# Optimization experiments

Hardware: AMD Instinct MI355X
Metric: run time of the kernel (lower is better)

The kernel has to match this reference:

```python
import jax, jax.numpy as jnp
import numpy as np

B, S, D = 8, 1024, 512          # batch, seq_len, embed_dim
H = 8                            # num_heads
KD = D                           # key_dim = embed_dim (per source)
DM = H * KD                      # internal d_model = 4096
FF = 2048                        # dense_dim
EPS = 1e-3                       # keras LayerNormalization default epsilon


def glorot(key, shape):
    fan_in, fan_out = shape[0], shape[1]
    lim = np.sqrt(6.0 / (fan_in + fan_out)).astype(np.float32)
    return jax.random.uniform(key, shape, jnp.float32, -lim, lim)


def setup_inputs() -> dict:
    key = jax.random.key(0)
    ks = jax.random.split(key, 8)
    return {
        "inputs": jax.random.normal(ks[0], (B, S, D), jnp.float32),
        "w_q": glorot(ks[1], (D, DM)), "b_q": jnp.zeros((DM,), jnp.float32),
        "w_k": glorot(ks[2], (D, DM)), "b_k": jnp.zeros((DM,), jnp.float32),
        "w_v": glorot(ks[3], (D, DM)), "b_v": jnp.zeros((DM,), jnp.float32),
        "w_o": glorot(ks[4], (DM, D)), "b_o": jnp.zeros((D,), jnp.float32),
        "w1": glorot(ks[5], (D, FF)), "b1": jnp.zeros((FF,), jnp.float32),
        "w2": glorot(ks[6], (FF, D)), "b2": jnp.zeros((D,), jnp.float32),
        "g1": jnp.ones((D,), jnp.float32), "beta1": jnp.zeros((D,), jnp.float32),
        "g2": jnp.ones((D,), jnp.float32), "beta2": jnp.zeros((D,), jnp.float32),
    }


def _layernorm(x, gamma, beta):
    mu = jnp.mean(x, axis=-1, keepdims=True)
    var = jnp.mean(jnp.square(x - mu), axis=-1, keepdims=True)
    return (x - mu) * jax.lax.rsqrt(var + EPS) * gamma + beta


def reference(inputs, w_q, b_q, w_k, b_k, w_v, b_v, w_o, b_o,
              w1, b1, w2, b2, g1, beta1, g2, beta2):
    # --- custom multi-head self-attention ---
    q = (inputs @ w_q + b_q).reshape(B, S, H, KD)   # [B,S,H,KD]
    k = (inputs @ w_k + b_k).reshape(B, S, H, KD)
    v = (inputs @ w_v + b_v).reshape(B, S, H, KD)
    scale = jnp.sqrt(jnp.float32(KD))
    scores = jnp.einsum("bqhd,bkhd->bhqk", q, k) / scale   # [B,H,S,S]
    attn = jax.nn.softmax(scores, axis=-1)
    ctx = jnp.einsum("bhqk,bkhd->bqhd", attn, v).reshape(B, S, DM)
    attn_out = ctx @ w_o + b_o                               # [B,S,D]
    # --- residual + LN 1 ---
    proj_in = _layernorm(inputs + attn_out, g1, beta1)
    # --- FFN ---
    ffn = jax.nn.relu(proj_in @ w1 + b1) @ w2 + b2
    # --- residual + LN 2 ---
    return _layernorm(proj_in + ffn, g2, beta2)
```

## Files before the change

### kernel.cpp

```cpp
#include <hip/hip_runtime.h>
#include <stdint.h>

typedef __bf16 bf16_t;
typedef bf16_t bf16x8 __attribute__((ext_vector_type(8)));
typedef float floatx4 __attribute__((ext_vector_type(4)));

__device__ __forceinline__ unsigned short f2bf(float f) {
  union { float f; uint32_t u; } v; v.f = f;
  return (unsigned short)((v.u + 0x7fffu + ((v.u >> 16) & 1u)) >> 16);
}

__device__ __forceinline__ float bf2f(unsigned short b) {
  union { uint32_t u; float f; } v;
  v.u = (uint32_t)b << 16;
  return v.f;
}

#define GLD16(g, l)                                                            \
  __builtin_amdgcn_global_load_lds(                                            \
      (const __attribute__((address_space(1))) void*)(g),                      \
      (__attribute__((address_space(3))) void*)(l), 16, 0, 0)

__device__ __forceinline__ void xcd_swizzle(int& bx, int& by) {
  const int nx = gridDim.x;
  const int nwg = nx * gridDim.y;
  int id = blockIdx.y * nx + blockIdx.x;
  const int cpx = nwg >> 3;
  id = (id & 7) * cpx + (id >> 3);
  bx = id % nx;
  by = id / nx;
}

template <int BIAS_MODE, bool RELU, bool OUT_BF16>
__global__ __launch_bounds__(512, 2) void gemm256(
    const unsigned short* __restrict__ A, const unsigned short* __restrict__ Bt,
    void* __restrict__ C, const float* __restrict__ bias, int K, int lda,
    int ldb, int ldc, long sA, long sB, long sC) {
  __shared__ __align__(16) unsigned short As[2][256 * 64];
  __shared__ __align__(16) unsigned short Bs[2][256 * 64];
  int bx, by;
  xcd_swizzle(bx, by);
  const int tid = threadIdx.x;
  const int lane = tid & 63;
  const int wave = tid >> 6;
  const int quad = lane >> 4;
  const int l15 = lane & 15;
  const unsigned short* Ab = A + blockIdx.z * sA + (long)by * 256 * lda;
  const unsigned short* Bb = Bt + blockIdx.z * sB + (long)bx * 256 * ldb;
  const int wm = (wave & 1) << 7;
  const int wn = (wave >> 1) << 6;

  floatx4 acc[8][4] = {};

  const int sr = tid >> 3;
  const int sc = tid & 7;
  const int NT = K >> 6;

  auto stage = [&](int t, int buf) {
    const int kt = t << 6;
#pragma unroll
    for (int i = 0; i < 4; ++i) {
      int r = sr + i * 64;
      int gc = sc ^ (r & 7);
      GLD16(Ab + (long)r * lda + kt + gc * 8,
            &As[buf][(i * 64 + (wave << 3)) * 64]);
    }
#pragma unroll
    for (int i = 0; i < 4; ++i) {
      int r = sr + i * 64;
      int gc = sc ^ (r & 7);
      GLD16(Bb + (long)r * ldb + kt + gc * 8,
            &Bs[buf][(i * 64 + (wave << 3)) * 64]);
    }
  };

  stage(0, 0);
  stage(1, 1);
  asm volatile("s_waitcnt vmcnt(8)\n\ts_barrier" ::: "memory");

  int cur = 0;
  for (int t = 0; t < NT; ++t) {
    const unsigned short* Ap = As[cur];
    const unsigned short* Bp = Bs[cur];
    bf16x8 bF[2][2][2];
#pragma unroll
    for (int jh = 0; jh < 2; ++jh)
#pragma unroll
      for (int j2 = 0; j2 < 2; ++j2)
#pragma unroll
        for (int ks = 0; ks < 2; ++ks) {
          int row = wn + jh * 32 + j2 * 16 + l15;
          int sw = (ks * 4 + quad) ^ (row & 7);
          bF[jh][j2][ks] = *(const bf16x8*)(Bp + row * 64 + sw * 8);
        }
#pragma unroll
    for (int ih = 0; ih < 2; ++ih) {
      bf16x8 aF[4][2];
#pragma unroll
      for (int i4 = 0; i4 < 4; ++i4)
#pragma unroll
        for (int ks = 0; ks < 2; ++ks) {
          int row = wm + ih * 64 + i4 * 16 + l15;
          int sw = (ks * 4 + quad) ^ (row & 7);
          aF[i4][ks] = *(const bf16x8*)(Ap + row * 64 + sw * 8);
        }
#pragma unroll
      for (int jh = 0; jh < 2; ++jh) {
        __builtin_amdgcn_s_setprio(1);
#pragma unroll
        for (int j2 = 0; j2 < 2; ++j2)
#pragma unroll
          for (int i4 = 0; i4 < 4; ++i4)
#pragma unroll
            for (int ks = 0; ks < 2; ++ks)
              acc[ih * 4 + i4][jh * 2 + j2] =
                  __builtin_amdgcn_mfma_f32_16x16x32_bf16(
                      aF[i4][ks], bF[jh][j2][ks],
                      acc[ih * 4 + i4][jh * 2 + j2], 0, 0, 0);
        __builtin_amdgcn_s_setprio(0);
      }
    }
    if (t == NT - 1) break;
    asm volatile("s_waitcnt lgkmcnt(0)\n\ts_barrier" ::: "memory");
    if (t + 2 < NT) {
      stage(t + 2, cur);
      asm volatile("s_waitcnt vmcnt(8)\n\ts_barrier" ::: "memory");
    } else {
      asm volatile("s_waitcnt vmcnt(0)\n\ts_barrier" ::: "memory");
    }
    cur ^= 1;
  }

  const int rl = quad << 2;
  const int cl = l15;
#pragma unroll
  for (int i = 0; i < 8; ++i) {
#pragma unroll
    for (int j = 0; j < 4; ++j) {
#pragma unroll
      for (int rg = 0; rg < 4; ++rg) {
        int row = (by << 8) + wm + i * 16 + rl + rg;
        int col = (bx << 8) + wn + j * 16 + cl;
        float v = acc[i][j][rg];
        if (BIAS_MODE == 1) v += bias[col];
        if (BIAS_MODE == 2) v += bias[row];
        if (RELU) v = fmaxf(v, 0.0f);
        long idx = blockIdx.z * sC + (long)row * ldc + col;
        if (OUT_BF16)
          ((unsigned short*)C)[idx] = f2bf(v);
        else
          ((float*)C)[idx] = v;
      }
    }
  }
}

template <int BIAS_MODE, bool RELU, bool OUT_BF16>
__global__ __launch_bounds__(256, 2) void gemm128p(
    const unsigned short* __restrict__ A, const unsigned short* __restrict__ Bt,
    void* __restrict__ C, const float* __restrict__ bias, int K, int lda,
    int ldb, int ldc, long sA, long sB, long sC) {
  __shared__ __align__(16) unsigned short As[2][128 * 64];
  __shared__ __align__(16) unsigned short Bs[2][128 * 64];
  int bx, by;
  xcd_swizzle(bx, by);
  const int tid = threadIdx.x;
  const int lane = tid & 63;
  const int wave = tid >> 6;
  const int quad = lane >> 4;
  const int l15 = lane & 15;
  const unsigned short* Ab = A + blockIdx.z * sA + (long)by * 128 * lda;
  const unsigned short* Bb = Bt + blockIdx.z * sB + (long)bx * 128 * ldb;
  const int wm = (wave & 1) << 6;
  const int wn = (wave >> 1) << 6;

  floatx4 acc[4][4] = {};

  const int sr = tid >> 3;
  const int sc = tid & 7;
  const int NT = K >> 6;

  auto stage = [&](int t, int buf) {
    const int kt = t << 6;
#pragma unroll
    for (int i = 0; i < 4; ++i) {
      int r = sr + i * 32;
      int gc = sc ^ (r & 7);
      GLD16(Ab + (long)r * lda + kt + gc * 8,
            &As[buf][(i * 32 + (wave << 3)) * 64]);
    }
#pragma unroll
    for (int i = 0; i < 4; ++i) {
      int r = sr + i * 32;
      int gc = sc ^ (r & 7);
      GLD16(Bb + (long)r * ldb + kt + gc * 8,
            &Bs[buf][(i * 32 + (wave << 3)) * 64]);
    }
  };

  stage(0, 0);
  stage(1, 1);
  asm volatile("s_waitcnt vmcnt(8)\n\ts_barrier" ::: "memory");

  int cur = 0;
  for (int t = 0; t < NT; ++t) {
    const unsigned short* Ap = As[cur];
    const unsigned short* Bp = Bs[cur];
#pragma unroll
    for (int ks = 0; ks < 2; ++ks) {
      bf16x8 af[4], bfr[4];
#pragma unroll
      for (int i = 0; i < 4; ++i) {
        int row = wm + i * 16 + l15;
        int ch = (ks * 4 + quad) ^ (row & 7);
        af[i] = *(const bf16x8*)(Ap + row * 64 + ch * 8);
      }
#pragma unroll
      for (int j = 0; j < 4; ++j) {
        int row = wn + j * 16 + l15;
        int ch = (ks * 4 + quad) ^ (row & 7);
        bfr[j] = *(const bf16x8*)(Bp + row * 64 + ch * 8);
      }
      __builtin_amdgcn_s_setprio(1);
#pragma unroll
      for (int i = 0; i < 4; ++i)
#pragma unroll
        for (int j = 0; j < 4; ++j)
          acc[i][j] = __builtin_amdgcn_mfma_f32_16x16x32_bf16(af[i], bfr[j],
                                                              acc[i][j], 0, 0, 0);
      __builtin_amdgcn_s_setprio(0);
    }
    if (t == NT - 1) break;
    asm volatile("s_waitcnt lgkmcnt(0)\n\ts_barrier" ::: "memory");
    if (t + 2 < NT) {
      stage(t + 2, cur);
      asm volatile("s_waitcnt vmcnt(8)\n\ts_barrier" ::: "memory");
    } else {
      asm volatile("s_waitcnt vmcnt(0)\n\ts_barrier" ::: "memory");
    }
    cur ^= 1;
  }

  const int rl = quad << 2;
  const int cl = l15;
#pragma unroll
  for (int i = 0; i < 4; ++i) {
#pragma unroll
    for (int j = 0; j < 4; ++j) {
#pragma unroll
      for (int rg = 0; rg < 4; ++rg) {
        int row = (by << 7) + wm + i * 16 + rl + rg;
        int col = (bx << 7) + wn + j * 16 + cl;
        float v = acc[i][j][rg];
        if (BIAS_MODE == 1) v += bias[col];
        if (BIAS_MODE == 2) v += bias[row];
        if (RELU) v = fmaxf(v, 0.0f);
        long idx = blockIdx.z * sC + (long)row * ldc + col;
        if (OUT_BF16)
          ((unsigned short*)C)[idx] = f2bf(v);
        else
          ((float*)C)[idx] = v;
      }
    }
  }
}

__global__ __launch_bounds__(512, 2) void attn(
    const unsigned short* __restrict__ qk, const unsigned short* __restrict__ vt,
    unsigned short* __restrict__ ctx) {
  __shared__ unsigned short ldsK[2][32 * 512];
  __shared__ unsigned short ldsV[2][32 * 512];
  __shared__ unsigned short ldsP[128 * 40];
  __shared__ float ldsL[128];

  const int tid = threadIdx.x;
  const int lane = tid & 63;
  const int wave = tid >> 6;
  const int quad = lane >> 4;
  const int l15 = lane & 15;
  const int b = blockIdx.x >> 3;
  const int h = blockIdx.x & 7;
  const int qblk = blockIdx.y << 7;
  const float cs = 0.044194173824159216f * 1.4426950408889634f;

  bf16x8 qf[16];
  {
    const unsigned short* qp =
        qk + (long)(b * 1024 + qblk + wave * 16 + l15) * 8192 + h * 512 +
        (quad << 3);
#pragma unroll
    for (int ks = 0; ks < 16; ++ks) qf[ks] = *(const bf16x8*)(qp + ks * 32);
  }

  floatx4 o[32];
#pragma unroll
  for (int i = 0; i < 32; ++i) o[i] = floatx4{0.f, 0.f, 0.f, 0.f};
  floatx4 l_i = floatx4{0.f, 0.f, 0.f, 0.f};

  const int st_d = lane >> 2;
  const int st_kc = ((lane & 3) - (lane >> 3)) & 3;

  {
#pragma unroll
    for (int i = 0; i < 4; ++i) {
      int r = i * 8 + wave;
      int gc = (lane & ~7) | ((lane ^ r) & 7);
      GLD16(qk + (long)(b * 1024 + r) * 8192 + 4096 + h * 512 + gc * 8,
            ldsK[0] + r * 512);
    }
#pragma unroll
    for (int i = 0; i < 4; ++i) {
      int j = i * 8 + wave;
      GLD16(vt + (long)(b * 4096 + h * 512 + j * 16 + st_d) * 1024 + st_kc * 8,
            ldsV[0] + j * 512);
    }
  }
  __syncthreads();

  for (int kt = 0; kt < 32; ++kt) {
    const unsigned short* kb = ldsK[kt & 1];
    const unsigned short* vb = ldsV[kt & 1];
    if (kt + 1 < 32) {
#pragma unroll
      for (int i = 0; i < 4; ++i) {
        int r = i * 8 + wave;
        int gc = (lane & ~7) | ((lane ^ r) & 7);
        GLD16(qk + (long)(b * 1024 + (kt + 1) * 32 + r) * 8192 + 4096 +
                  h * 512 + gc * 8,
              ldsK[(kt + 1) & 1] + r * 512);
      }
#pragma unroll
      for (int i = 0; i < 4; ++i) {
        int j = i * 8 + wave;
        GLD16(vt + (long)(b * 4096 + h * 512 + j * 16 + st_d) * 1024 +
                  (kt + 1) * 32 + st_kc * 8,
              ldsV[(kt + 1) & 1] + j * 512);
      }
    }

    floatx4 s0 = floatx4{0.f, 0.f, 0.f, 0.f}, s1 = floatx4{0.f, 0.f, 0.f, 0.f};
#pragma unroll
    for (int ks = 0; ks < 16; ++ks) {
      int ch = ks * 4 + quad;
      int sw = (ch & ~7) | ((ch ^ l15) & 7);
      bf16x8 k0 = *(const bf16x8*)(kb + l15 * 512 + sw * 8);
      bf16x8 k1 = *(const bf16x8*)(kb + (16 + l15) * 512 + sw * 8);
      s0 = __builtin_amdgcn_mfma_f32_16x16x32_bf16(qf[ks], k0, s0, 0, 0, 0);
      s1 = __builtin_amdgcn_mfma_f32_16x16x32_bf16(qf[ks], k1, s1, 0, 0, 0);
    }

    {
      unsigned short* pw = ldsP + wave * 16 * 40;
      const int rb = quad << 2;
#pragma unroll
      for (int r = 0; r < 4; ++r) {
        float e0 = __builtin_amdgcn_exp2f(s0[r] * cs);
        float e1 = __builtin_amdgcn_exp2f(s1[r] * cs);
        l_i[r] += e0 + e1;
        pw[(rb + r) * 40 + l15] = f2bf(e0);
        pw[(rb + r) * 40 + 16 + l15] = f2bf(e1);
      }
    }
    asm volatile("s_waitcnt lgkmcnt(0)\n\ts_barrier" ::: "memory");

#pragma unroll
    for (int half = 0; half < 2; ++half) {
      bf16x8 pf[4];
#pragma unroll
      for (int q4 = 0; q4 < 4; ++q4)
        pf[q4] = *(const bf16x8*)(ldsP + ((half * 4 + q4) * 16 + l15) * 40 +
                                  (quad << 3));
#pragma unroll
      for (int db = 0; db < 4; ++db) {
        int n = wave * 4 + db;
        bf16x8 vf = *(const bf16x8*)(
            vb + n * 512 + (l15 * 4 + ((quad + (l15 >> 1)) & 3)) * 8);
#pragma unroll
        for (int q4 = 0; q4 < 4; ++q4)
          o[(half * 4 + q4) * 4 + db] = __builtin_amdgcn_mfma_f32_16x16x32_bf16(
              pf[q4], vf, o[(half * 4 + q4) * 4 + db], 0, 0, 0);
      }
    }
    __syncthreads();
  }

#pragma unroll
  for (int r = 0; r < 4; ++r) {
    float rs = l_i[r];
    rs += __shfl_xor(rs, 1);
    rs += __shfl_xor(rs, 2);
    rs += __shfl_xor(rs, 4);
    rs += __shfl_xor(rs, 8);
    if (l15 == 0) ldsL[wave * 16 + (quad << 2) + r] = rs;
  }
  __syncthreads();

#pragma unroll
  for (int qb = 0; qb < 8; ++qb) {
    floatx4 lv = *(const floatx4*)(ldsL + qb * 16 + (quad << 2));
    floatx4 inv;
#pragma unroll
    for (int r = 0; r < 4; ++r) inv[r] = 1.0f / lv[r];
#pragma unroll
    for (int db = 0; db < 4; ++db) {
#pragma unroll
      for (int r = 0; r < 4; ++r) {
        long row = (long)(b * 1024 + qblk + qb * 16 + (quad << 2) + r);
        ctx[row * 4096 + h * 512 + wave * 64 + db * 16 + l15] =
            f2bf(o[qb * 4 + db][r] * inv[r]);
      }
    }
  }
}

template <int NPART, bool WB>
__global__ __launch_bounds__(256) void ln_reduce(
    const unsigned short* __restrict__ p, long sP,
    const float* __restrict__ bias, const float* __restrict__ resid,
    const float* __restrict__ gamma, const float* __restrict__ beta,
    float* __restrict__ of, unsigned short* __restrict__ ob) {
  const long row = blockIdx.x;
  const int c = threadIdx.x * 2;
  const float2 rv = ((const float2*)(resid + row * 512))[threadIdx.x];
  float x0 = bias[c] + rv.x;
  float x1 = bias[c + 1] + rv.y;
#pragma unroll
  for (int k = 0; k < NPART; ++k) {
    const ushort2 a = ((const ushort2*)(p + k * sP + row * 512))[threadIdx.x];
    x0 += bf2f(a.x);
    x1 += bf2f(a.y);
  }
  float s = x0 + x1;
  float ss = x0 * x0 + x1 * x1;
#pragma unroll
  for (int d = 1; d < 64; d <<= 1) {
    s += __shfl_xor(s, d);
    ss += __shfl_xor(ss, d);
  }
  __shared__ float ps[4], pq[4];
  const int wave = threadIdx.x >> 6;
  if ((threadIdx.x & 63) == 0) {
    ps[wave] = s;
    pq[wave] = ss;
  }
  __syncthreads();
  s = ps[0] + ps[1] + ps[2] + ps[3];
  ss = pq[0] + pq[1] + pq[2] + pq[3];
  const float mu = s * (1.0f / 512.0f);
  const float rstd = rsqrtf(ss * (1.0f / 512.0f) - mu * mu + 1e-3f);
  const float y0 = (x0 - mu) * rstd * gamma[c] + beta[c];
  const float y1 = (x1 - mu) * rstd * gamma[c + 1] + beta[c + 1];
  ((float2*)(of + row * 512))[threadIdx.x] = make_float2(y0, y1);
  if (WB) {
    ushort2 o2;
    o2.x = f2bf(y0);
    o2.y = f2bf(y1);
    ((ushort2*)(ob + row * 512))[threadIdx.x] = o2;
  }
}

__global__ __launch_bounds__(256) void cast_bf16(const float* __restrict__ in,
                                                 unsigned short* __restrict__ out,
                                                 int n) {
  int i = (blockIdx.x * 256 + threadIdx.x) * 4;
  if (i < n) {
    float4 v = *(const float4*)(in + i);
    ushort4 o;
    o.x = f2bf(v.x);
    o.y = f2bf(v.y);
    o.z = f2bf(v.z);
    o.w = f2bf(v.w);
    *(ushort4*)(out + i) = o;
  }
}

__global__ __launch_bounds__(256) void transpose_cast(const float* __restrict__ in,
                                                      unsigned short* __restrict__ out,
                                                      int R, int C) {
  __shared__ float tile[32][33];
  const int tx = threadIdx.x & 31, ty = threadIdx.x >> 5;
  const int c0 = blockIdx.x * 32, r0 = blockIdx.y * 32;
#pragma unroll
  for (int i = 0; i < 4; ++i)
    tile[ty + i * 8][tx] = in[(long)(r0 + ty + i * 8) * C + c0 + tx];
  __syncthreads();
#pragma unroll
  for (int i = 0; i < 4; ++i)
    out[(long)(c0 + ty + i * 8) * R + r0 + tx] = f2bf(tile[tx][ty + i * 8]);
}

extern "C" void kernel_launch(void* const* d_in, const int* in_sizes, int n_in,
                              void* d_out, int out_size, void* d_ws,
                              size_t ws_size, hipStream_t stream) {
  const float* x = (const float*)d_in[0];
  const float* w_q = (const float*)d_in[1];
  const float* b_q = (const float*)d_in[2];
  const float* w_k = (const float*)d_in[3];
  const float* b_k = (const float*)d_in[4];
  const float* w_v = (const float*)d_in[5];
  const float* b_v = (const float*)d_in[6];
  const float* w_o = (const float*)d_in[7];
  const float* b_o = (const float*)d_in[8];
  const float* w1 = (const float*)d_in[9];
  const float* b1 = (const float*)d_in[10];
  const float* w2 = (const float*)d_in[11];
  const float* b2 = (const float*)d_in[12];
  const float* g1 = (const float*)d_in[13];
  const float* be1 = (const float*)d_in[14];
  const float* g2 = (const float*)d_in[15];
  const float* be2 = (const float*)d_in[16];
  float* out = (float*)d_out;

  char* ws = (char*)d_ws;
  size_t off = 0;
  auto alloc = [&](size_t n) {
    char* p = ws + off;
    off += (n + 255) & ~(size_t)255;
    return p;
  };
  unsigned short* xb = (unsigned short*)alloc(8192ll * 512 * 2);
  unsigned short* wqk_t = (unsigned short*)alloc(8192ll * 512 * 2);
  unsigned short* wv_t = (unsigned short*)alloc(4096ll * 512 * 2);
  unsigned short* wo_t = (unsigned short*)alloc(512ll * 4096 * 2);
  unsigned short* w1_t = (unsigned short*)alloc(2048ll * 512 * 2);
  unsigned short* w2_t = (unsigned short*)alloc(512ll * 2048 * 2);
  float* bqk = (float*)alloc(8192ll * 4);
  unsigned short* qkb = (unsigned short*)alloc(4096ll * 8192 * 2);
  unsigned short* vtb = (unsigned short*)alloc(8ll * 4096 * 1024 * 2);
  unsigned short* ctxf = (unsigned short*)alloc(8192ll * 4096 * 2);
  float* proj = (float*)alloc(8192ll * 512 * 4);
  unsigned short* projb = xb;
  unsigned short* h1 = qkb;
  unsigned short* pOP = qkb;
  unsigned short* pF2 = (unsigned short*)ctxf;

  hipMemcpyAsync(bqk, b_q, 4096 * 4, hipMemcpyDeviceToDevice, stream);
  hipMemcpyAsync(bqk + 4096, b_k, 4096 * 4, hipMemcpyDeviceToDevice, stream);

  cast_bf16<<<4096, 256, 0, stream>>>(x, xb, 8192 * 512);
  transpose_cast<<<dim3(128, 16), 256, 0, stream>>>(w_q, wqk_t, 512, 4096);
  transpose_cast<<<dim3(128, 16), 256, 0, stream>>>(w_k, wqk_t + 4096ll * 512, 512, 4096);
  transpose_cast<<<dim3(128, 16), 256, 0, stream>>>(w_v, wv_t, 512, 4096);
  transpose_cast<<<dim3(16, 128), 256, 0, stream>>>(w_o, wo_t, 4096, 512);
  transpose_cast<<<dim3(64, 16), 256, 0, stream>>>(w1, w1_t, 512, 2048);
  transpose_cast<<<dim3(16, 64), 256, 0, stream>>>(w2, w2_t, 2048, 512);

  gemm256<2, false, true><<<dim3(4, 16, 8), 512, 0, stream>>>(
      wv_t, xb, vtb, b_v, 512, 512, 512, 1024, 0, 1024ll * 512,
      4096ll * 1024);

  for (int g = 0; g < 2; ++g) {
    const unsigned short* xg = xb + (long)g * 4096 * 512;
    gemm256<1, false, true><<<dim3(32, 16, 1), 512, 0, stream>>>(
        xg, wqk_t, qkb, bqk, 512, 512, 512, 8192, 0, 0, 0);
    attn<<<dim3(32, 8), 512, 0, stream>>>(
        qkb, vtb + (long)g * 4 * 4096 * 1024, ctxf + (long)g * 4096 * 4096);
  }
  gemm128p<0, false, true><<<dim3(4, 64, 2), 256, 0, stream>>>(
      ctxf, wo_t, pOP, nullptr, 2048, 4096, 4096, 512, 2048, 2048,
      8192ll * 512);
  ln_reduce<2, true><<<8192, 256, 0, stream>>>(pOP, 8192ll * 512, b_o, x, g1,
                                               be1, proj, projb);
  gemm256<1, true, true><<<dim3(8, 32, 1), 512, 0, stream>>>(
      projb, w1_t, h1, b1, 512, 512, 512, 2048, 0, 0, 0);
  gemm128p<0, false, true><<<dim3(4, 64, 2), 256, 0, stream>>>(
      h1, w2_t, pF2, nullptr, 1024, 2048, 2048, 512, 1024, 1024,
      8192ll * 512);
  ln_reduce<2, false><<<8192, 256, 0, stream>>>(pF2, 8192ll * 512, b2, proj,
                                                g2, be2, out, nullptr);
}
```

Baseline: 473.2 us.

## Interleave LDS prefetch with MFMA quadrants in GEMM main loop

Restructures the 256x256 GEMM K-loop into four MFMA quadrants. LDS fragment loads for the second half are issued between compute phases, and the global-to-LDS staging of the next-next tile for A and B is issued in the middle of the last two quadrants instead of after all compute. The aim is to hide global and LDS latency behind matrix-core work in a ping-pong style schedule. It adds extra barriers per iteration and keeps more fragment registers live. The buffer being refilled must not still be read by slower waves, and the added barriers are meant to guarantee that.

```diff
diff --git a/kernel.cpp b/kernel.cpp
--- a/kernel.cpp
+++ b/kernel.cpp
@@ -56,7 +56,7 @@
   const int sc = tid & 7;
   const int NT = K >> 6;
 
-  auto stage = [&](int t, int buf) {
+  auto stageA = [&](int t, int buf) {
     const int kt = t << 6;
 #pragma unroll
     for (int i = 0; i < 4; ++i) {
@@ -65,6 +65,9 @@
       GLD16(Ab + (long)r * lda + kt + gc * 8,
             &As[buf][(i * 64 + (wave << 3)) * 64]);
     }
+  };
+  auto stageB = [&](int t, int buf) {
+    const int kt = t << 6;
 #pragma unroll
     for (int i = 0; i < 4; ++i) {
       int r = sr + i * 64;
@@ -74,60 +77,107 @@
     }
   };
 
-  stage(0, 0);
-  stage(1, 1);
+  stageA(0, 0);
+  stageB(0, 0);
+  stageA(1, 1);
+  stageB(1, 1);
   asm volatile("s_waitcnt vmcnt(8)\n\ts_barrier" ::: "memory");
 
   int cur = 0;
   for (int t = 0; t < NT; ++t) {
     const unsigned short* Ap = As[cur];
     const unsigned short* Bp = Bs[cur];
-    bf16x8 bF[2][2][2];
-#pragma unroll
-    for (int jh = 0; jh < 2; ++jh)
-#pragma unroll
-      for (int j2 = 0; j2 < 2; ++j2)
-#pragma unroll
-        for (int ks = 0; ks < 2; ++ks) {
-          int row = wn + jh * 32 + j2 * 16 + l15;
-          int sw = (ks * 4 + quad) ^ (row & 7);
-          bF[jh][j2][ks] = *(const bf16x8*)(Bp + row * 64 + sw * 8);
-        }
-#pragma unroll
-    for (int ih = 0; ih < 2; ++ih) {
-      bf16x8 aF[4][2];
+    bf16x8 aF0[4][2], aF1[4][2], bF[2][2][2];
+
+#pragma unroll
+    for (int j2 = 0; j2 < 2; ++j2)
+#pragma unroll
+      for (int ks = 0; ks < 2; ++ks) {
+        int row = wn + j2 * 16 + l15;
+        int sw = (ks * 4 + quad) ^ (row & 7);
+        bF[0][j2][ks] = *(const bf16x8*)(Bp + row * 64 + sw * 8);
+      }
+#pragma unroll
+    for (int i4 = 0; i4 < 4; ++i4)
+#pragma unroll
+      for (int ks = 0; ks < 2; ++ks) {
+        int row = wm + i4 * 16 + l15;
+        int sw = (ks * 4 + quad) ^ (row & 7);
+        aF0[i4][ks] = *(const bf16x8*)(Ap + row * 64 + sw * 8);
+      }
+    __builtin_amdgcn_s_barrier();
+    asm volatile("s_waitcnt lgkmcnt(0)" ::: "memory");
+    __builtin_amdgcn_s_setprio(1);
+#pragma unroll
+    for (int j2 = 0; j2 < 2; ++j2)
 #pragma unroll
       for (int i4 = 0; i4 < 4; ++i4)
 #pragma unroll
-        for (int ks = 0; ks < 2; ++ks) {
-          int row = wm + ih * 64 + i4 * 16 + l15;
-          int sw = (ks * 4 + quad) ^ (row & 7);
-          aF[i4][ks] = *(const bf16x8*)(Ap + row * 64 + sw * 8);
-        }
-#pragma unroll
-      for (int jh = 0; jh < 2; ++jh) {
-        __builtin_amdgcn_s_setprio(1);
-#pragma unroll
-        for (int j2 = 0; j2 < 2; ++j2)
-#pragma unroll
-          for (int i4 = 0; i4 < 4; ++i4)
-#pragma unroll
-            for (int ks = 0; ks < 2; ++ks)
-              acc[ih * 4 + i4][jh * 2 + j2] =
-                  __builtin_amdgcn_mfma_f32_16x16x32_bf16(
-                      aF[i4][ks], bF[jh][j2][ks],
-                      acc[ih * 4 + i4][jh * 2 + j2], 0, 0, 0);
-        __builtin_amdgcn_s_setprio(0);
-      }
-    }
+        for (int ks = 0; ks < 2; ++ks)
+          acc[i4][j2] = __builtin_amdgcn_mfma_f32_16x16x32_bf16(
+              aF0[i4][ks], bF[0][j2][ks], acc[i4][j2], 0, 0, 0);
+    __builtin_amdgcn_s_setprio(0);
+    __builtin_amdgcn_s_barrier();
+
+#pragma unroll
+    for (int j2 = 0; j2 < 2; ++j2)
+#pragma unroll
+      for (int ks = 0; ks < 2; ++ks) {
+        int row = wn + 32 + j2 * 16 + l15;
+        int sw = (ks * 4 + quad) ^ (row & 7);
+        bF[1][j2][ks] = *(const bf16x8*)(Bp + row * 64 + sw * 8);
+      }
+#pragma unroll
+    for (int i4 = 0; i4 < 4; ++i4)
+#pragma unroll
+      for (int ks = 0; ks < 2; ++ks) {
+        int row = wm + 64 + i4 * 16 + l15;
+        int sw = (ks * 4 + quad) ^ (row & 7);
+        aF1[i4][ks] = *(const bf16x8*)(Ap + row * 64 + sw * 8);
+      }
+    __builtin_amdgcn_s_barrier();
+    asm volatile("s_waitcnt lgkmcnt(0)" ::: "memory");
+    __builtin_amdgcn_s_setprio(1);
+#pragma unroll
+    for (int j2 = 0; j2 < 2; ++j2)
+#pragma unroll
+      for (int i4 = 0; i4 < 4; ++i4)
+#pragma unroll
+        for (int ks = 0; ks < 2; ++ks)
+          acc[i4][2 + j2] = __builtin_amdgcn_mfma_f32_16x16x32_bf16(
+              aF0[i4][ks], bF[1][j2][ks], acc[i4][2 + j2], 0, 0, 0);
+    __builtin_amdgcn_s_setprio(0);
+    __builtin_amdgcn_s_barrier();
+
+    if (t + 2 < NT) stageA(t + 2, cur);
+    __builtin_amdgcn_s_setprio(1);
+#pragma unroll
+    for (int j2 = 0; j2 < 2; ++j2)
+#pragma unroll
+      for (int i4 = 0; i4 < 4; ++i4)
+#pragma unroll
+        for (int ks = 0; ks < 2; ++ks)
+          acc[4 + i4][j2] = __builtin_amdgcn_mfma_f32_16x16x32_bf16(
+              aF1[i4][ks], bF[0][j2][ks], acc[4 + i4][j2], 0, 0, 0);
+    __builtin_amdgcn_s_setprio(0);
+
+    if (t + 2 < NT) stageB(t + 2, cur);
+    __builtin_amdgcn_s_setprio(1);
+#pragma unroll
+    for (int j2 = 0; j2 < 2; ++j2)
+#pragma unroll
+      for (int i4 = 0; i4 < 4; ++i4)
+#pragma unroll
+        for (int ks = 0; ks < 2; ++ks)
+          acc[4 + i4][2 + j2] = __builtin_amdgcn_mfma_f32_16x16x32_bf16(
+              aF1[i4][ks], bF[1][j2][ks], acc[4 + i4][2 + j2], 0, 0, 0);
+    __builtin_amdgcn_s_setprio(0);
+
     if (t == NT - 1) break;
-    asm volatile("s_waitcnt lgkmcnt(0)\n\ts_barrier" ::: "memory");
-    if (t + 2 < NT) {
-      stage(t + 2, cur);
+    if (t + 2 < NT)
       asm volatile("s_waitcnt vmcnt(8)\n\ts_barrier" ::: "memory");
-    } else {
+    else
       asm volatile("s_waitcnt vmcnt(0)\n\ts_barrier" ::: "memory");
-    }
     cur ^= 1;
   }
 
```

After: 469.5 us. No clear change (-0.8%).
